# Performance work log

Hardware: AMD Instinct MI355X
Metric: run time of the kernel (lower is better)

Reference implementation:

```python
import jax, jax.numpy as jnp
import numpy as np

B, S, E = 4, 2048, 1024
H, D = 16, 64  # num_heads, head_size; H*D == E


def setup_inputs() -> dict:
    key = jax.random.key(0)
    ks = jax.random.split(key, 6)
    scale = E ** -0.5
    x = jax.random.normal(ks[0], (B, S, E), dtype=jnp.float32)
    # per-head bias-free q/k/v projections, stacked over heads: [H, E, D]
    Wq = jax.random.normal(ks[1], (H, E, D), dtype=jnp.float32) * scale
    Wk = jax.random.normal(ks[2], (H, E, D), dtype=jnp.float32) * scale
    Wv = jax.random.normal(ks[3], (H, E, D), dtype=jnp.float32) * scale
    # output projection: Linear(H*D, E) with bias
    Wproj = jax.random.normal(ks[4], (H * D, E), dtype=jnp.float32) * ((H * D) ** -0.5)
    bproj = jax.random.normal(ks[5], (E,), dtype=jnp.float32) * 0.01
    return {"x": x, "Wq": Wq, "Wk": Wk, "Wv": Wv, "Wproj": Wproj, "bproj": bproj}


def reference(x, Wq, Wk, Wv, Wproj, bproj):
    # Batched equivalent of the per-head loop: each head h computes
    # q = x @ Wq[h], k = x @ Wk[h], v = x @ Wv[h]
    q = jnp.einsum("bse,hed->bhsd", x, Wq)
    k = jnp.einsum("bse,hed->bhsd", x, Wk)
    v = jnp.einsum("bse,hed->bhsd", x, Wv)
    # causal scaled dot-product attention, scale = head_size**-0.5
    scores = jnp.einsum("bhqd,bhkd->bhqk", q, k) * (D ** -0.5)
    causal = jnp.tril(jnp.ones((S, S), dtype=bool))  # [S, S]
    scores = jnp.where(causal, scores, jnp.finfo(scores.dtype).min)
    attn = jax.nn.softmax(scores, axis=-1)  # dropout = identity in eval
    out = jnp.einsum("bhqk,bhkd->bhqd", attn, v)
    # concat heads along the feature dim, then project (dropout = identity)
    out = out.transpose(0, 2, 1, 3).reshape(B, S, H * D)
    return out @ Wproj + bproj
```

## Files before the change

kernel.cpp:

```cpp
#include <hip/hip_runtime.h>
#include <stdint.h>

typedef unsigned short u16;
typedef __attribute__((ext_vector_type(8))) short bf16x8;
typedef __attribute__((ext_vector_type(8))) unsigned short u16x8;
typedef __attribute__((ext_vector_type(4))) float f32x4;

#define S_LEN 2048
#define EDIM 1024
#define NH 16
#define HD 64

static __device__ __forceinline__ u16 f2bf(float f) {
  union { float f; uint32_t u; } v; v.f = f;
  uint32_t r = v.u + 0x7fffu + ((v.u >> 16) & 1u);
  return (u16)(r >> 16);
}

static __device__ __forceinline__ uint32_t cvtpk_bf16(float a, float b) {
  uint32_t r;
  asm("v_cvt_pk_bf16_f32 %0, %1, %2" : "=v"(r) : "v"(a), "v"(b));
  return r;
}

static __device__ __forceinline__ void gload_lds16(const u16* g, u16* l) {
  __builtin_amdgcn_global_load_lds(
      (const __attribute__((address_space(1))) void*)g,
      (__attribute__((address_space(3))) void*)l, 16, 0, 0);
}

static __device__ __forceinline__ bf16x8 gload16(const u16* p) {
  bf16x8 r;
  asm volatile("global_load_dwordx4 %0, %1, off" : "=v"(r) : "v"(p));
  return r;
}

#define WAIT_VM(n)                                   \
  do {                                               \
    asm volatile("s_waitcnt vmcnt(" #n ")");         \
    __builtin_amdgcn_sched_barrier(0);               \
  } while (0)

#define BARRIER()                                    \
  do {                                               \
    __builtin_amdgcn_s_barrier();                    \
    __builtin_amdgcn_sched_barrier(0);               \
  } while (0)

__global__ __launch_bounds__(256) void pack_inputs(
    const float* __restrict__ x, const float* __restrict__ Wq,
    const float* __restrict__ Wk, const float* __restrict__ Wv,
    const float* __restrict__ Wp,
    u16* __restrict__ xb, u16* __restrict__ wqkvT, u16* __restrict__ wprojT) {
  const int blk = blockIdx.x;
  const int tid = threadIdx.x;
  if (blk < 8192) {
    int idx = blk * 256 + tid;
    float4 v = ((const float4*)x)[idx];
    ushort4 o;
    o.x = f2bf(v.x); o.y = f2bf(v.y); o.z = f2bf(v.z); o.w = f2bf(v.w);
    ((ushort4*)xb)[idx] = o;
    return;
  }
  __shared__ u16 tile[64][65];
  const float* src;
  size_t src_rs;
  u16* dst;
  float wscale = 1.0f;
  if (blk < 8960) {
    int t = blk - 8192;
    int mh = t >> 4;
    int et = t & 15;
    int m = mh >> 4, h = mh & 15;
    const float* W = (m == 0) ? Wq : (m == 1) ? Wk : Wv;
    if (m == 0) wscale = 0.1803368801111204f;
    src = W + ((size_t)(h * EDIM + et * 64)) * HD;
    src_rs = HD;
    dst = wqkvT + (size_t)(m * 1024 + h * 64) * 1024 + et * 64;
  } else {
    int t = blk - 8960;
    int kt = t >> 4, nt = t & 15;
    src = Wp + (size_t)(kt * 64) * 1024 + nt * 64;
    src_rs = 1024;
    dst = wprojT + (size_t)(nt * 64) * 1024 + kt * 64;
  }
  {
    const int rr = tid >> 4;
    const int c4 = (tid & 15) << 2;
#pragma unroll
    for (int p = 0; p < 4; p++) {
      const int r = p * 16 + rr;
      float4 v = *(const float4*)(src + (size_t)r * src_rs + c4);
      tile[r][c4 + 0] = f2bf(v.x * wscale);
      tile[r][c4 + 1] = f2bf(v.y * wscale);
      tile[r][c4 + 2] = f2bf(v.z * wscale);
      tile[r][c4 + 3] = f2bf(v.w * wscale);
    }
  }
  __syncthreads();
  {
    const int rr = tid >> 3;
    const int c8 = (tid & 7) << 3;
#pragma unroll
    for (int p = 0; p < 2; p++) {
      const int r = p * 32 + rr;
      u16x8 o;
#pragma unroll
      for (int j = 0; j < 8; j++) o[j] = tile[c8 + j][r];
      *(u16x8*)(dst + (size_t)r * 1024 + c8) = o;
    }
  }
}

template <int EPI>
__global__ __launch_bounds__(256) void gemm128(
    const u16* __restrict__ A, const u16* __restrict__ Bt,
    const float* __restrict__ bias,
    u16* __restrict__ o0, u16* __restrict__ o1, u16* __restrict__ o2,
    float* __restrict__ of, int K, int N) {
  __shared__ __align__(16) u16 As[128 * 64];
  __shared__ __align__(16) u16 Bs[128 * 64];
  const int tid  = threadIdx.x;
  const int lane = tid & 63;
  const int wave = tid >> 6;
  const int wm = wave >> 1;
  const int wn = wave & 1;
  const int col = lane & 15;
  const int quad = lane >> 4;
  const int cs = col & 7;
  const int m0 = blockIdx.y << 7;
  const int n0 = blockIdx.x << 7;

  const int srow  = lane >> 3;
  const int sslot = (lane & 7) ^ srow;
  const u16* gA = A + (size_t)(m0 + (wave << 5) + srow) * K + sslot * 8;
  const u16* gB = Bt + (size_t)(n0 + (wave << 5) + srow) * K + sslot * 8;
  u16* lA = &As[(wave << 5) << 6];
  u16* lB = &Bs[(wave << 5) << 6];

  f32x4 acc[4][4];
#pragma unroll
  for (int i = 0; i < 4; i++)
#pragma unroll
    for (int j = 0; j < 4; j++) acc[i][j] = (f32x4){0.f, 0.f, 0.f, 0.f};

  for (int kk = 0; kk < K; kk += 64) {
    __syncthreads();
#pragma unroll
    for (int i = 0; i < 4; i++) {
      gload_lds16(gA + (size_t)(i * 8) * K + kk, lA + i * 512);
      gload_lds16(gB + (size_t)(i * 8) * K + kk, lB + i * 512);
    }
    __syncthreads();

#pragma unroll
    for (int x = 0; x < 2; x++) {
      bf16x8 af[4], bfr[4];
#pragma unroll
      for (int i = 0; i < 4; i++)
        af[i] = *(const bf16x8*)(
            &As[((wm * 64 + i * 16 + col) << 6) + ((((x << 2) + quad) ^ cs) << 3)]);
#pragma unroll
      for (int j = 0; j < 4; j++)
        bfr[j] = *(const bf16x8*)(
            &Bs[((wn * 64 + j * 16 + col) << 6) + ((((x << 2) + quad) ^ cs) << 3)]);
#pragma unroll
      for (int i = 0; i < 4; i++)
#pragma unroll
        for (int j = 0; j < 4; j++)
          acc[i][j] = __builtin_amdgcn_mfma_f32_16x16x32_bf16(af[i], bfr[j],
                                                              acc[i][j], 0, 0, 0);
    }
  }

#pragma unroll
  for (int i = 0; i < 4; i++) {
#pragma unroll
    for (int j = 0; j < 4; j++) {
      const int rg0 = m0 + wm * 64 + i * 16 + quad * 4;
      const int cg = n0 + wn * 64 + j * 16 + col;
      if (EPI == 0) {
        const int mat = cg >> 10;
        const int rem = cg & 1023;
        const int h = rem >> 6;
        const int d = rem & 63;
        const int b = rg0 >> 11;
        const int s0 = rg0 & 2047;
        if (mat == 2) {
          ushort4 o;
          o.x = f2bf(acc[i][j][0]); o.y = f2bf(acc[i][j][1]);
          o.z = f2bf(acc[i][j][2]); o.w = f2bf(acc[i][j][3]);
          *(ushort4*)(&o2[(((size_t)(b * NH + h) * HD + d) << 11) + s0]) = o;
        } else {
          u16* dst = (mat == 0) ? o0 : o1;
#pragma unroll
          for (int r = 0; r < 4; r++)
            dst[((size_t)((b * NH + h) * S_LEN + s0 + r) << 6) + d] =
                f2bf(acc[i][j][r]);
        }
      } else {
#pragma unroll
        for (int r = 0; r < 4; r++)
          of[(size_t)(rg0 + r) * N + cg] = acc[i][j][r] + bias[cg];
      }
    }
  }
}

__global__ __launch_bounds__(256, 3) void attn_fused(
    const u16* __restrict__ Q, const u16* __restrict__ K,
    const u16* __restrict__ Vt, u16* __restrict__ O) {
  __shared__ __align__(16) u16 Kbuf[2][64 * 64];
  __shared__ __align__(16) u16 Vbuf[2][64 * 64];
  __shared__ __align__(16) u16 Ps[4][2][16 * 72];

  const int tid  = threadIdx.x;
  const int lane = tid & 63;
  const int wave = tid >> 6;
  const int col  = lane & 15;
  const int quad = lane >> 4;
  const int cs   = col & 7;
  const int gid  = blockIdx.x;
  const int bh = ((gid & 7) << 3) | ((gid >> 3) & 7);
  const int qb = 15 - (gid >> 6);
  const int b = bh >> 4;
  const int h = bh & 15;
  const int q0w = qb * 128 + wave * 32;

  const u16* Kbh = K + (size_t)bh * S_LEN * HD;
  const u16* Vbh = Vt + (size_t)bh * HD * S_LEN;

  const int srow  = lane >> 3;
  const int sslot = (lane & 7) ^ srow;
  const int r0a = wave * 16;
  const int r0b = wave * 16 + 8;

  bf16x8 qf[2][2];
#pragma unroll
  for (int a = 0; a < 2; a++) {
    const u16* Qrow = Q + ((size_t)bh * S_LEN + q0w + a * 16 + col) * HD;
    qf[a][0] = gload16(Qrow + quad * 8);
    qf[a][1] = gload16(Qrow + 32 + quad * 8);
  }

  f32x4 oacc[2][4];
#pragma unroll
  for (int a = 0; a < 2; a++)
#pragma unroll
    for (int n = 0; n < 4; n++) oacc[a][n] = (f32x4){0.f, 0.f, 0.f, 0.f};
  float lrow[2][4] = {{0.f, 0.f, 0.f, 0.f}, {0.f, 0.f, 0.f, 0.f}};

  auto STAGE = [&](int buf, int kv0) {
    gload_lds16(Kbh + (size_t)(kv0 + r0a + srow) * HD + sslot * 8,
                &Kbuf[buf][r0a * 64]);
    gload_lds16(Kbh + (size_t)(kv0 + r0b + srow) * HD + sslot * 8,
                &Kbuf[buf][r0b * 64]);
    gload_lds16(Vbh + (size_t)(r0a + srow) * S_LEN + kv0 + sslot * 8,
                &Vbuf[buf][r0a * 64]);
    gload_lds16(Vbh + (size_t)(r0b + srow) * S_LEN + kv0 + sslot * 8,
                &Vbuf[buf][r0b * 64]);
  };

  const int T = 2 * qb + 2;
  int cur = 0;
  STAGE(0, 0);
  WAIT_VM(0);
  BARRIER();

  for (int t = 0; t < T; t++) {
    const int kv0 = t << 6;
    if (t + 1 < T) STAGE(cur ^ 1, kv0 + 64);

    if (kv0 <= q0w + 31) {
      f32x4 sc[2][4];
#pragma unroll
      for (int j = 0; j < 4; j++) {
        const u16* kr = &Kbuf[cur][(j * 16 + col) * 64];
        const bf16x8 kf0 = *(const bf16x8*)(kr + ((quad ^ cs) << 3));
        const bf16x8 kf1 = *(const bf16x8*)(kr + (((4 + quad) ^ cs) << 3));
#pragma unroll
        for (int a = 0; a < 2; a++) {
          sc[a][j] = (f32x4){0.f, 0.f, 0.f, 0.f};
          sc[a][j] = __builtin_amdgcn_mfma_f32_16x16x32_bf16(qf[a][0], kf0, sc[a][j], 0, 0, 0);
          sc[a][j] = __builtin_amdgcn_mfma_f32_16x16x32_bf16(qf[a][1], kf1, sc[a][j], 0, 0, 0);
        }
      }

      const bool diag = (kv0 + 63 > q0w);
#pragma unroll
      for (int a = 0; a < 2; a++)
#pragma unroll
        for (int r = 0; r < 4; r++) {
          float p[4];
#pragma unroll
          for (int j = 0; j < 4; j++) {
            float v = exp2f(sc[a][j][r]);
            if (diag) {
              const int ql = q0w - kv0 + a * 16 + quad * 4 + r;
              if (j * 16 + col > ql) v = 0.f;
            }
            lrow[a][r] += v;
            p[j] = v;
          }
          const uint32_t pk0 = cvtpk_bf16(p[0], p[1]);
          const uint32_t pk1 = cvtpk_bf16(p[2], p[3]);
          u16* row = &Ps[wave][a][(quad * 4 + r) * 72 + col];
          row[0]  = (u16)pk0;
          row[16] = (u16)(pk0 >> 16);
          row[32] = (u16)pk1;
          row[48] = (u16)(pk1 >> 16);
        }
      bf16x8 pf[2][2];
#pragma unroll
      for (int a = 0; a < 2; a++) {
        pf[a][0] = *(const bf16x8*)(&Ps[wave][a][col * 72 + quad * 8]);
        pf[a][1] = *(const bf16x8*)(&Ps[wave][a][col * 72 + 32 + quad * 8]);
      }

#pragma unroll
      for (int n = 0; n < 4; n++) {
        const u16* vr = &Vbuf[cur][(n * 16 + col) * 64];
        const bf16x8 vf0 = *(const bf16x8*)(vr + ((quad ^ cs) << 3));
        const bf16x8 vf1 = *(const bf16x8*)(vr + (((4 + quad) ^ cs) << 3));
#pragma unroll
        for (int a = 0; a < 2; a++) {
          oacc[a][n] = __builtin_amdgcn_mfma_f32_16x16x32_bf16(pf[a][0], vf0, oacc[a][n], 0, 0, 0);
          oacc[a][n] = __builtin_amdgcn_mfma_f32_16x16x32_bf16(pf[a][1], vf1, oacc[a][n], 0, 0, 0);
        }
      }
    }

    WAIT_VM(0);
    BARRIER();
    cur ^= 1;
  }

#pragma unroll
  for (int a = 0; a < 2; a++)
#pragma unroll
    for (int r = 0; r < 4; r++) {
      float l = lrow[a][r];
#pragma unroll
      for (int off = 1; off < 16; off <<= 1) l += __shfl_xor(l, off);
      const float inv = 1.0f / l;
      const size_t row = (size_t)b * S_LEN + q0w + a * 16 + quad * 4 + r;
#pragma unroll
      for (int n = 0; n < 4; n++)
        O[row * EDIM + h * HD + n * 16 + col] = f2bf(oacc[a][n][r] * inv);
    }
}

extern "C" void kernel_launch(void* const* d_in, const int* in_sizes, int n_in,
                              void* d_out, int out_size, void* d_ws, size_t ws_size,
                              hipStream_t stream) {
  const float* x  = (const float*)d_in[0];
  const float* Wq = (const float*)d_in[1];
  const float* Wk = (const float*)d_in[2];
  const float* Wv = (const float*)d_in[3];
  const float* Wp = (const float*)d_in[4];
  const float* bp = (const float*)d_in[5];
  float* out = (float*)d_out;

  char* ws = (char*)d_ws;
  u16* wqkvT  = (u16*)(ws);
  u16* wprojT = (u16*)(ws + 6291456);
  u16* Qb     = (u16*)(ws + 8388608);
  u16* Kb     = (u16*)(ws + 25165824);
  u16* Vtb    = (u16*)(ws + 41943040);
  u16* xb     = (u16*)(ws + 58720256);
  u16* Ob     = xb;

  pack_inputs<<<dim3(9216), dim3(256), 0, stream>>>(x, Wq, Wk, Wv, Wp,
                                                    xb, wqkvT, wprojT);
  gemm128<0><<<dim3(24, 64), dim3(256), 0, stream>>>(
      xb, wqkvT, (const float*)nullptr, Qb, Kb, Vtb, (float*)nullptr, 1024, 3072);
  attn_fused<<<dim3(1024), dim3(256), 0, stream>>>(Qb, Kb, Vtb, Ob);
  gemm128<1><<<dim3(8, 64), dim3(256), 0, stream>>>(
      Ob, wprojT, bp, (u16*)nullptr, (u16*)nullptr, (u16*)nullptr, out, 1024, 1024);
}
```

Before: 268.2 us.

## Switch attention to transposed 32x32x16 MFMA and keep P in registers

Rewrites the attention inner loop to compute S^T with 32x32x16 bf16 MFMAs (K as the A operand, Q as B), so each lane owns one query row. The probabilities are then repacked across half-waves with shuffles and fed directly as the B operand of the PV MFMA, which removes the per-wave LDS P staging buffer and its store/load round trip. Row sums need only one cross-lane shuffle at the end, and the output is written with vectorized ushort4 stores. Launch bounds rise to 4 blocks per CU, which tightens the register budget and adds a risk of spills.

```diff
diff --git a/kernel.cpp b/kernel.cpp
--- a/kernel.cpp
+++ b/kernel.cpp
@@ -5,6 +5,7 @@
 typedef __attribute__((ext_vector_type(8))) short bf16x8;
 typedef __attribute__((ext_vector_type(8))) unsigned short u16x8;
 typedef __attribute__((ext_vector_type(4))) float f32x4;
+typedef __attribute__((ext_vector_type(16))) float f32x16;
 
 #define S_LEN 2048
 #define EDIM 1024
@@ -207,19 +208,17 @@
   }
 }
 
-__global__ __launch_bounds__(256, 3) void attn_fused(
+__global__ __launch_bounds__(256, 4) void attn_fused(
     const u16* __restrict__ Q, const u16* __restrict__ K,
     const u16* __restrict__ Vt, u16* __restrict__ O) {
   __shared__ __align__(16) u16 Kbuf[2][64 * 64];
   __shared__ __align__(16) u16 Vbuf[2][64 * 64];
-  __shared__ __align__(16) u16 Ps[4][2][16 * 72];
 
   const int tid  = threadIdx.x;
   const int lane = tid & 63;
   const int wave = tid >> 6;
-  const int col  = lane & 15;
-  const int quad = lane >> 4;
-  const int cs   = col & 7;
+  const int q31  = lane & 31;
+  const int hi   = lane >> 5;
   const int gid  = blockIdx.x;
   const int bh = ((gid & 7) << 3) | ((gid >> 3) & 7);
   const int qb = 15 - (gid >> 6);
@@ -235,20 +234,21 @@
   const int r0a = wave * 16;
   const int r0b = wave * 16 + 8;
 
-  bf16x8 qf[2][2];
-#pragma unroll
-  for (int a = 0; a < 2; a++) {
-    const u16* Qrow = Q + ((size_t)bh * S_LEN + q0w + a * 16 + col) * HD;
-    qf[a][0] = gload16(Qrow + quad * 8);
-    qf[a][1] = gload16(Qrow + 32 + quad * 8);
-  }
-
-  f32x4 oacc[2][4];
-#pragma unroll
-  for (int a = 0; a < 2; a++)
-#pragma unroll
-    for (int n = 0; n < 4; n++) oacc[a][n] = (f32x4){0.f, 0.f, 0.f, 0.f};
-  float lrow[2][4] = {{0.f, 0.f, 0.f, 0.f}, {0.f, 0.f, 0.f, 0.f}};
+  const int qs = q31 & 7;
+
+  bf16x8 qf[4];
+  {
+    const u16* Qrow = Q + ((size_t)bh * S_LEN + q0w + q31) * HD;
+#pragma unroll
+    for (int m = 0; m < 4; m++) qf[m] = gload16(Qrow + (((m << 1) + hi) << 3));
+  }
+
+  f32x16 oacc[2];
+#pragma unroll
+  for (int db = 0; db < 2; db++)
+#pragma unroll
+    for (int r = 0; r < 16; r++) oacc[db][r] = 0.f;
+  float lacc = 0.f;
 
   auto STAGE = [&](int buf, int kv0) {
     gload_lds16(Kbh + (size_t)(kv0 + r0a + srow) * HD + sslot * 8,
@@ -272,60 +272,56 @@
     if (t + 1 < T) STAGE(cur ^ 1, kv0 + 64);
 
     if (kv0 <= q0w + 31) {
-      f32x4 sc[2][4];
-#pragma unroll
-      for (int j = 0; j < 4; j++) {
-        const u16* kr = &Kbuf[cur][(j * 16 + col) * 64];
-        const bf16x8 kf0 = *(const bf16x8*)(kr + ((quad ^ cs) << 3));
-        const bf16x8 kf1 = *(const bf16x8*)(kr + (((4 + quad) ^ cs) << 3));
-#pragma unroll
-        for (int a = 0; a < 2; a++) {
-          sc[a][j] = (f32x4){0.f, 0.f, 0.f, 0.f};
-          sc[a][j] = __builtin_amdgcn_mfma_f32_16x16x32_bf16(qf[a][0], kf0, sc[a][j], 0, 0, 0);
-          sc[a][j] = __builtin_amdgcn_mfma_f32_16x16x32_bf16(qf[a][1], kf1, sc[a][j], 0, 0, 0);
+      f32x16 sct[2];
+#pragma unroll
+      for (int cb = 0; cb < 2; cb++) {
+#pragma unroll
+        for (int r = 0; r < 16; r++) sct[cb][r] = 0.f;
+        const u16* kr = &Kbuf[cur][((cb << 5) + q31) * 64];
+#pragma unroll
+        for (int m = 0; m < 4; m++) {
+          const bf16x8 kf = *(const bf16x8*)(kr + ((((m << 1) + hi) ^ qs) << 3));
+          sct[cb] = __builtin_amdgcn_mfma_f32_32x32x16_bf16(kf, qf[m], sct[cb], 0, 0, 0);
         }
       }
 
+      uint32_t pk[2][8];
       const bool diag = (kv0 + 63 > q0w);
-#pragma unroll
-      for (int a = 0; a < 2; a++)
-#pragma unroll
-        for (int r = 0; r < 4; r++) {
-          float p[4];
-#pragma unroll
-          for (int j = 0; j < 4; j++) {
-            float v = exp2f(sc[a][j][r]);
-            if (diag) {
-              const int ql = q0w - kv0 + a * 16 + quad * 4 + r;
-              if (j * 16 + col > ql) v = 0.f;
-            }
-            lrow[a][r] += v;
-            p[j] = v;
+      const int qg = q0w + q31;
+#pragma unroll
+      for (int cb = 0; cb < 2; cb++) {
+#pragma unroll
+        for (int u = 0; u < 8; u++) {
+          float p0 = exp2f(sct[cb][2 * u]);
+          float p1 = exp2f(sct[cb][2 * u + 1]);
+          if (diag) {
+            const int k0 = kv0 + (cb << 5) + ((2 * u) & 3) + 8 * (u >> 1) + 4 * hi;
+            if (k0 > qg) p0 = 0.f;
+            if (k0 + 1 > qg) p1 = 0.f;
           }
-          const uint32_t pk0 = cvtpk_bf16(p[0], p[1]);
-          const uint32_t pk1 = cvtpk_bf16(p[2], p[3]);
-          u16* row = &Ps[wave][a][(quad * 4 + r) * 72 + col];
-          row[0]  = (u16)pk0;
-          row[16] = (u16)(pk0 >> 16);
-          row[32] = (u16)pk1;
-          row[48] = (u16)(pk1 >> 16);
+          lacc += p0 + p1;
+          pk[cb][u] = cvtpk_bf16(p0, p1);
         }
-      bf16x8 pf[2][2];
-#pragma unroll
-      for (int a = 0; a < 2; a++) {
-        pf[a][0] = *(const bf16x8*)(&Ps[wave][a][col * 72 + quad * 8]);
-        pf[a][1] = *(const bf16x8*)(&Ps[wave][a][col * 72 + 32 + quad * 8]);
-      }
-
-#pragma unroll
-      for (int n = 0; n < 4; n++) {
-        const u16* vr = &Vbuf[cur][(n * 16 + col) * 64];
-        const bf16x8 vf0 = *(const bf16x8*)(vr + ((quad ^ cs) << 3));
-        const bf16x8 vf1 = *(const bf16x8*)(vr + (((4 + quad) ^ cs) << 3));
-#pragma unroll
-        for (int a = 0; a < 2; a++) {
-          oacc[a][n] = __builtin_amdgcn_mfma_f32_16x16x32_bf16(pf[a][0], vf0, oacc[a][n], 0, 0, 0);
-          oacc[a][n] = __builtin_amdgcn_mfma_f32_16x16x32_bf16(pf[a][1], vf1, oacc[a][n], 0, 0, 0);
+      }
+
+#pragma unroll
+      for (int m = 0; m < 4; m++) {
+        const int cb = m >> 1;
+        const int bb = (m & 1) << 2;
+        const uint32_t x0 = (uint32_t)__shfl_xor((int)pk[cb][bb + 0], 32);
+        const uint32_t x1 = (uint32_t)__shfl_xor((int)pk[cb][bb + 1], 32);
+        const uint32_t x2 = (uint32_t)__shfl_xor((int)pk[cb][bb + 2], 32);
+        const uint32_t x3 = (uint32_t)__shfl_xor((int)pk[cb][bb + 3], 32);
+        union { uint32_t u[4]; bf16x8 v; } P;
+        P.u[0] = hi ? x2 : pk[cb][bb + 0];
+        P.u[1] = hi ? x3 : pk[cb][bb + 1];
+        P.u[2] = hi ? pk[cb][bb + 2] : x0;
+        P.u[3] = hi ? pk[cb][bb + 3] : x1;
+#pragma unroll
+        for (int db = 0; db < 2; db++) {
+          const bf16x8 vf = *(const bf16x8*)(
+              &Vbuf[cur][((db << 5) + q31) * 64 + ((((m << 1) + hi) ^ qs) << 3)]);
+          oacc[db] = __builtin_amdgcn_mfma_f32_32x32x16_bf16(vf, P.v, oacc[db], 0, 0, 0);
         }
       }
     }
@@ -335,19 +331,23 @@
     cur ^= 1;
   }
 
-#pragma unroll
-  for (int a = 0; a < 2; a++)
-#pragma unroll
-    for (int r = 0; r < 4; r++) {
-      float l = lrow[a][r];
-#pragma unroll
-      for (int off = 1; off < 16; off <<= 1) l += __shfl_xor(l, off);
-      const float inv = 1.0f / l;
-      const size_t row = (size_t)b * S_LEN + q0w + a * 16 + quad * 4 + r;
-#pragma unroll
-      for (int n = 0; n < 4; n++)
-        O[row * EDIM + h * HD + n * 16 + col] = f2bf(oacc[a][n][r] * inv);
-    }
+  {
+    const float l = lacc + __shfl_xor(lacc, 32);
+    const float inv = 1.0f / l;
+    const size_t row = (size_t)b * S_LEN + q0w + q31;
+#pragma unroll
+    for (int db = 0; db < 2; db++)
+#pragma unroll
+      for (int g = 0; g < 4; g++) {
+        const int d0 = (db << 5) + (g << 3) + (hi << 2);
+        ushort4 o;
+        o.x = f2bf(oacc[db][g * 4 + 0] * inv);
+        o.y = f2bf(oacc[db][g * 4 + 1] * inv);
+        o.z = f2bf(oacc[db][g * 4 + 2] * inv);
+        o.w = f2bf(oacc[db][g * 4 + 3] * inv);
+        *(ushort4*)(&O[row * EDIM + h * HD + d0]) = o;
+      }
+  }
 }
 
 extern "C" void kernel_launch(void* const* d_in, const int* in_sizes, int n_in,
```

Measured after the change: 267.4 us. No clear change (-0.3%).
